# Kernel optimization log

Hardware: AMD Instinct MI355X
Metric: run time of the kernel (lower is better)

Reference implementation:

```python
import jax, jax.numpy as jnp
import numpy as np

TEMP = 1.0  # composition softmax temperature

def _bank_topk(x, U, V, logits, top_k):
    # softmax over primitive logits, select top-k, renormalize, fused low-rank projection
    w = jax.nn.softmax(logits / TEMP)                     # [P]
    tw, ti = jax.lax.top_k(w, top_k)                      # [k], [k]
    tw = tw / tw.sum()
    Us = U[ti]                                            # [k, d_in, r]
    Vs = V[ti]                                            # [k, r, d_out]
    h = jnp.einsum('bsd,kdr->bksr', x, Us)                # low-rank bottleneck
    return jnp.einsum('bksr,kro,k->bso', h, Vs, tw)       # weighted fuse

def reference(x, q_U, q_V, k_U, k_V, v_U, v_V, q_logits, k_logits, v_logits, out_w, top_k):
    B, S, _ = x.shape
    H, D = 16, 64
    q = _bank_topk(x, q_U, q_V, q_logits, top_k)
    k = _bank_topk(x, k_U, k_V, k_logits, top_k)
    v = _bank_topk(x, v_U, v_V, v_logits, top_k)
    q = q.reshape(B, S, H, D).transpose(0, 2, 1, 3)       # [B,H,S,D]
    k = k.reshape(B, S, H, D).transpose(0, 2, 1, 3)
    v = v.reshape(B, S, H, D).transpose(0, 2, 1, 3)
    scale = 1.0 / jnp.sqrt(jnp.asarray(D, dtype=x.dtype))
    scores = jnp.einsum('bhqd,bhkd->bhqk', q, k) * scale  # [B,H,S,S]
    causal = jnp.triu(jnp.ones((S, S), dtype=bool), 1)
    scores = jnp.where(causal[None, None], jnp.finfo(x.dtype).min, scores)
    probs = jax.nn.softmax(scores, axis=-1)
    out = jnp.einsum('bhqk,bhkd->bhqd', probs, v)
    out = out.transpose(0, 2, 1, 3).reshape(B, S, H * D)
    return out @ out_w.T                                   # nn.Linear(H*D, d_model, bias=False)

def setup_inputs() -> dict:
    key = jax.random.key(0)
    ks = jax.random.split(key, 11)
    P, d, r = 16, 1024, 64
    B, S = 4, 1024
    f = jnp.float32
    inp = {
        'x': jax.random.normal(ks[0], (B, S, d), f),
        'q_U': jax.random.normal(ks[1], (P, d, r), f) * (1.0 / np.sqrt(d)),
        'q_V': jax.random.normal(ks[2], (P, r, d), f) * (1.0 / np.sqrt(r)),
        'k_U': jax.random.normal(ks[3], (P, d, r), f) * (1.0 / np.sqrt(d)),
        'k_V': jax.random.normal(ks[4], (P, r, d), f) * (1.0 / np.sqrt(r)),
        'v_U': jax.random.normal(ks[5], (P, d, r), f) * (1.0 / np.sqrt(d)),
        'v_V': jax.random.normal(ks[6], (P, r, d), f) * (1.0 / np.sqrt(r)),
        'q_logits': jax.random.normal(ks[7], (P,), f) * 0.01,
        'k_logits': jax.random.normal(ks[8], (P,), f) * 0.01,
        'v_logits': jax.random.normal(ks[9], (P,), f) * 0.01,
        'out_w': jax.random.normal(ks[10], (d, d), f) * (1.0 / np.sqrt(d)),
        'top_k': 4,
    }
    return inp
```

## Files before the change

### kernel.cpp

```cpp
#include <hip/hip_runtime.h>
#include <math.h>

#define D_MODEL 1024
#define RANK    64
#define PMAX    16
#define S_LEN   1024
#define HD      64
#define MROWS   4096
#define NHEAD   16
#define BATCH   4

typedef short short8v __attribute__((ext_vector_type(8)));
typedef float floatx4 __attribute__((ext_vector_type(4)));

typedef __attribute__((address_space(1))) const unsigned int* gptr_t;
typedef __attribute__((address_space(3))) unsigned int* lptr_t;

static __device__ __forceinline__ void async16(const void* g, void* l) {
    __builtin_amdgcn_global_load_lds((gptr_t)g, (lptr_t)l, 16, 0, 0);
}

static __device__ __forceinline__ short f2bf(float f) {
    unsigned int u = __float_as_uint(f);
    u = (u + 0x7fffu + ((u >> 16) & 1u)) >> 16;
    return (short)u;
}

__global__ void topk_weights_kernel(const float* __restrict__ ql,
                                    const float* __restrict__ kl,
                                    const float* __restrict__ vl,
                                    const int* __restrict__ topk,
                                    int* __restrict__ idx_out,
                                    float* __restrict__ w_out) {
    int bank = threadIdx.x;
    if (bank >= 3) return;
    const float* lg = (bank == 0) ? ql : (bank == 1) ? kl : vl;
    int K = *topk; if (K < 1) K = 1; if (K > PMAX) K = PMAX;
    float l[PMAX];
    for (int i = 0; i < PMAX; ++i) l[i] = lg[i];
    bool used[PMAX];
    for (int i = 0; i < PMAX; ++i) used[i] = false;
    int   sel_i[PMAX];
    float sel_l[PMAX];
    for (int j = 0; j < K; ++j) {
        int best = -1; float bv = -INFINITY;
        for (int i = 0; i < PMAX; ++i)
            if (!used[i] && l[i] > bv) { bv = l[i]; best = i; }
        used[best] = true; sel_i[j] = best; sel_l[j] = bv;
    }
    float mx = sel_l[0];
    float e[PMAX];
    float sum = 0.f;
    for (int j = 0; j < K; ++j) { e[j] = __expf(sel_l[j] - mx); sum += e[j]; }
    float inv = 1.f / sum;
    for (int j = 0; j < PMAX; ++j) {
        idx_out[bank * PMAX + j] = (j < K) ? sel_i[j] : 0;
        w_out[bank * PMAX + j]   = (j < K) ? e[j] * inv : 0.f;
    }
}

__global__ __launch_bounds__(256) void convert_bf16_kernel(
    const float* __restrict__ src, short* __restrict__ dst, int n4) {
    int i = blockIdx.x * 256 + threadIdx.x;
    if (i < n4) {
        float4 f = ((const float4*)src)[i];
        short4 o;
        o.x = f2bf(f.x); o.y = f2bf(f.y); o.z = f2bf(f.z); o.w = f2bf(f.w);
        ((short4*)dst)[i] = o;
    }
}

__global__ __launch_bounds__(256) void prep_uv_kernel(
    const float* __restrict__ qU, const float* __restrict__ kU,
    const float* __restrict__ vU,
    const float* __restrict__ qV, const float* __restrict__ kV,
    const float* __restrict__ vV,
    const int* __restrict__ idx, const float* __restrict__ wsel,
    const int* __restrict__ topk,
    short* __restrict__ Ut, short* __restrict__ Vt) {
    int z    = blockIdx.z;
    int j    = blockIdx.y;
    int tile = blockIdx.x;
    int t    = threadIdx.x;
    int K = *topk; if (K < 1) K = 1; if (K > PMAX) K = PMAX;
    if (j >= K) return;
    __shared__ float T[64][65];
    int bank = (z < 3) ? z : z - 3;
    int p = idx[bank * PMAX + j];

    if (z < 3) {
        const float* U = (bank == 0) ? qU : (bank == 1) ? kU : vU;
        const float* src = U + (size_t)p * D_MODEL * RANK;
        int d0 = tile * 64;
        int rl = t & 63, dq = t >> 6;
#pragma unroll
        for (int i = 0; i < 16; ++i) {
            int dl = i * 4 + dq;
            T[rl][dl] = src[(size_t)(d0 + dl) * RANK + rl];
        }
        __syncthreads();
        short* dst = Ut + (size_t)bank * D_MODEL * D_MODEL;
        int rr = t >> 2;
#pragma unroll
        for (int i = 0; i < 4; ++i) {
            int c = (t & 3) * 16 + i * 4;
            short4 o;
            o.x = f2bf(T[rr][c + 0]); o.y = f2bf(T[rr][c + 1]);
            o.z = f2bf(T[rr][c + 2]); o.w = f2bf(T[rr][c + 3]);
            *(short4*)&dst[(size_t)(j * 64 + rr) * D_MODEL + d0 + c] = o;
        }
    } else {
        const float* V = (bank == 0) ? qV : (bank == 1) ? kV : vV;
        float wj = wsel[bank * PMAX + j];
        const float* src = V + (size_t)p * RANK * D_MODEL;
        int n0 = tile * 64;
        int nl = t & 63, rq = t >> 6;
#pragma unroll
        for (int i = 0; i < 16; ++i) {
            int rl = i * 4 + rq;
            T[nl][rl] = src[(size_t)rl * D_MODEL + n0 + nl] * wj;
        }
        __syncthreads();
        short* dst = Vt + (size_t)bank * D_MODEL * D_MODEL;
        int rr = t >> 2;
#pragma unroll
        for (int i = 0; i < 4; ++i) {
            int c = (t & 3) * 16 + i * 4;
            short4 o;
            o.x = f2bf(T[rr][c + 0]); o.y = f2bf(T[rr][c + 1]);
            o.z = f2bf(T[rr][c + 2]); o.w = f2bf(T[rr][c + 3]);
            *(short4*)&dst[(size_t)(n0 + rr) * D_MODEL + j * 64 + c] = o;
        }
    }
}

static __device__ __forceinline__ void mfma_gemm_tile(
    const short* __restrict__ A, const short* __restrict__ B, int kl,
    int m0, int n0, short* As, short* Bs, floatx4 acc[4][4]) {
    const int t    = threadIdx.x;
    const int w    = t >> 6;
    const int lane = t & 63;
    const int wm   = w & 1, wn = w >> 1;
    const int colL = lane & 15, quad = lane >> 4;
    const int srow  = lane >> 2;
    const int skoff = (lane & 3) * 8;

#pragma unroll
    for (int i = 0; i < 4; ++i)
#pragma unroll
        for (int j = 0; j < 4; ++j) acc[i][j] = (floatx4){0.f, 0.f, 0.f, 0.f};

    for (int k0 = 0; k0 < kl; k0 += 32) {
        async16(A + (size_t)(m0 + w * 16 + srow) * D_MODEL + k0 + skoff,
                As + (w * 16 + srow) * 32 + skoff);
        async16(A + (size_t)(m0 + 64 + w * 16 + srow) * D_MODEL + k0 + skoff,
                As + (64 + w * 16 + srow) * 32 + skoff);
        async16(B + (size_t)(n0 + w * 16 + srow) * D_MODEL + k0 + skoff,
                Bs + (w * 16 + srow) * 32 + skoff);
        async16(B + (size_t)(n0 + 64 + w * 16 + srow) * D_MODEL + k0 + skoff,
                Bs + (64 + w * 16 + srow) * 32 + skoff);
        __syncthreads();
        short8v af[4], bf[4];
#pragma unroll
        for (int i = 0; i < 4; ++i)
            af[i] = *(const short8v*)&As[(wm * 64 + i * 16 + colL) * 32 + quad * 8];
#pragma unroll
        for (int j = 0; j < 4; ++j)
            bf[j] = *(const short8v*)&Bs[(wn * 64 + j * 16 + colL) * 32 + quad * 8];
#pragma unroll
        for (int i = 0; i < 4; ++i)
#pragma unroll
            for (int j = 0; j < 4; ++j)
                acc[i][j] = __builtin_amdgcn_mfma_f32_16x16x32_bf16(af[i], bf[j], acc[i][j], 0, 0, 0);
        __syncthreads();
    }
}

__global__ __launch_bounds__(256) void gemm_h_kernel(
    const short* __restrict__ xb, const short* __restrict__ Ut,
    const int* __restrict__ topk, short* __restrict__ h) {
    int K = *topk; if (K < 1) K = 1; if (K > PMAX) K = PMAX;
    int n0 = blockIdx.y * 128;
    if (n0 >= K * 64) return;
    int m0 = blockIdx.x * 128;
    int bank = blockIdx.z;
    __shared__ short As[128 * 32];
    __shared__ short Bs[128 * 32];
    floatx4 acc[4][4];
    mfma_gemm_tile(xb, Ut + (size_t)bank * D_MODEL * D_MODEL, D_MODEL, m0, n0, As, Bs, acc);

    const int t = threadIdx.x, w = t >> 6, lane = t & 63;
    const int wm = w & 1, wn = w >> 1, colL = lane & 15, quad = lane >> 4;
    short* H = h + (size_t)bank * MROWS * D_MODEL;
#pragma unroll
    for (int i = 0; i < 4; ++i)
#pragma unroll
        for (int j = 0; j < 4; ++j)
#pragma unroll
            for (int r = 0; r < 4; ++r)
                H[(size_t)(m0 + wm * 64 + i * 16 + quad * 4 + r) * D_MODEL +
                  (n0 + wn * 64 + j * 16 + colL)] = f2bf(acc[i][j][r]);
}

__global__ __launch_bounds__(256) void gemm_qkv_kernel(
    const short* __restrict__ h, const short* __restrict__ Vt,
    const int* __restrict__ topk, short* __restrict__ qkv) {
    int K = *topk; if (K < 1) K = 1; if (K > PMAX) K = PMAX;
    int m0 = blockIdx.x * 128;
    int n0 = blockIdx.y * 128;
    int bank = blockIdx.z;
    __shared__ short As[128 * 32];
    __shared__ short Bs[128 * 32];
    floatx4 acc[4][4];
    mfma_gemm_tile(h + (size_t)bank * MROWS * D_MODEL,
                   Vt + (size_t)bank * D_MODEL * D_MODEL, K * 64, m0, n0, As, Bs, acc);

    const int t = threadIdx.x, w = t >> 6, lane = t & 63;
    const int wm = w & 1, wn = w >> 1, colL = lane & 15, quad = lane >> 4;
    short* outp = qkv + (size_t)bank * MROWS * D_MODEL;
#pragma unroll
    for (int i = 0; i < 4; ++i)
#pragma unroll
        for (int j = 0; j < 4; ++j)
#pragma unroll
            for (int r = 0; r < 4; ++r) {
                int m = m0 + wm * 64 + i * 16 + quad * 4 + r;
                int n = n0 + wn * 64 + j * 16 + colL;
                int b = m >> 10, s = m & 1023;
                int head = n >> 6, d = n & 63;
                outp[(((size_t)(b * NHEAD + head) << 10) + s) * HD + d] = f2bf(acc[i][j][r]);
            }
}

__global__ __launch_bounds__(256) void gemm_proj_kernel(
    const short* __restrict__ attnb, const short* __restrict__ wb,
    float* __restrict__ outp) {
    int m0 = blockIdx.x * 128;
    int n0 = blockIdx.y * 128;
    __shared__ short As[128 * 32];
    __shared__ short Bs[128 * 32];
    floatx4 acc[4][4];
    mfma_gemm_tile(attnb, wb, D_MODEL, m0, n0, As, Bs, acc);

    const int t = threadIdx.x, w = t >> 6, lane = t & 63;
    const int wm = w & 1, wn = w >> 1, colL = lane & 15, quad = lane >> 4;
#pragma unroll
    for (int i = 0; i < 4; ++i)
#pragma unroll
        for (int j = 0; j < 4; ++j)
#pragma unroll
            for (int r = 0; r < 4; ++r)
                outp[(size_t)(m0 + wm * 64 + i * 16 + quad * 4 + r) * D_MODEL +
                     (n0 + wn * 64 + j * 16 + colL)] = acc[i][j][r];
}

__global__ __launch_bounds__(256) void attn_mfma_kernel(
    const short* __restrict__ qkv,
    short* __restrict__ attn_out) {
    const int t    = threadIdx.x;
    const int w    = t >> 6;
    const int lane = t & 63;
    const int col  = lane & 15;
    const int quad = lane >> 4;
    const int pr   = blockIdx.x;
    const int bh   = blockIdx.y;
    const size_t HS   = (size_t)S_LEN * HD;
    const size_t BSTR = (size_t)MROWS * D_MODEL;
    const short* Qg = qkv + (size_t)bh * HS;
    const short* Kg = qkv + BSTR + (size_t)bh * HS;
    const short* Vg = qkv + 2 * BSTR + (size_t)bh * HS;

    __shared__ short Ks[64][72];
    __shared__ short Vt[64][72];
    __shared__ short Ps[4][16][72];

    const float SC = 0.125f * 1.44269504f;

    for (int ph = 0; ph < 2; ++ph) {
        const int qt = ph ? (15 - pr) : pr;
        const int qrow = qt * 64 + w * 16 + col;
        short8v aq0 = *(const short8v*)(Qg + (size_t)qrow * HD + quad * 8);
        short8v aq1 = *(const short8v*)(Qg + (size_t)qrow * HD + 32 + quad * 8);
        floatx4 O0 = {0.f, 0.f, 0.f, 0.f}, O1 = O0, O2 = O0, O3 = O0;
        float mrow[4] = {-INFINITY, -INFINITY, -INFINITY, -INFINITY};
        float lrow[4] = {0.f, 0.f, 0.f, 0.f};

        for (int jt = 0; jt <= qt; ++jt) {
            __syncthreads();
            {
                int c = t;
                int key = c >> 3, db = (c & 7) * 8;
                *(short8v*)&Ks[key][db] =
                    *(const short8v*)(Kg + (size_t)(jt * 64 + key) * HD + db);
                c = t + 256;
                key = c >> 3; db = (c & 7) * 8;
                *(short8v*)&Ks[key][db] =
                    *(const short8v*)(Kg + (size_t)(jt * 64 + key) * HD + db);
            }
            {
                int k0 = (t & 31) * 2;
                int db = (t >> 5) * 8;
                short8v v0 = *(const short8v*)(Vg + (size_t)(jt * 64 + k0) * HD + db);
                short8v v1 = *(const short8v*)(Vg + (size_t)(jt * 64 + k0 + 1) * HD + db);
#pragma unroll
                for (int i = 0; i < 8; ++i) {
                    unsigned int pk = (unsigned int)(unsigned short)v0[i] |
                                      ((unsigned int)(unsigned short)v1[i] << 16);
                    *(unsigned int*)&Vt[db + i][k0] = pk;
                }
            }
            __syncthreads();

            const bool diag = (jt == qt);
            const int  nmax = diag ? w : 3;
            float sc[4][4];
#pragma unroll
            for (int n = 0; n < 4; ++n) {
                if (n <= nmax) {
                    floatx4 c4 = {0.f, 0.f, 0.f, 0.f};
                    short8v b0 = *(const short8v*)&Ks[n * 16 + col][quad * 8];
                    short8v b1 = *(const short8v*)&Ks[n * 16 + col][32 + quad * 8];
                    c4 = __builtin_amdgcn_mfma_f32_16x16x32_bf16(aq0, b0, c4, 0, 0, 0);
                    c4 = __builtin_amdgcn_mfma_f32_16x16x32_bf16(aq1, b1, c4, 0, 0, 0);
#pragma unroll
                    for (int r = 0; r < 4; ++r) {
                        float v = c4[r] * SC;
                        if (diag && n == w && col > quad * 4 + r) v = -INFINITY;
                        sc[n][r] = v;
                    }
                } else {
#pragma unroll
                    for (int r = 0; r < 4; ++r) sc[n][r] = -INFINITY;
                }
            }
            float pv[4][4];
#pragma unroll
            for (int r = 0; r < 4; ++r) {
                float tm = fmaxf(fmaxf(sc[0][r], sc[1][r]), fmaxf(sc[2][r], sc[3][r]));
                tm = fmaxf(tm, __shfl_xor(tm, 1));
                tm = fmaxf(tm, __shfl_xor(tm, 2));
                tm = fmaxf(tm, __shfl_xor(tm, 4));
                tm = fmaxf(tm, __shfl_xor(tm, 8));
                float mnew  = fmaxf(mrow[r], tm);
                float alpha = exp2f(mrow[r] - mnew);
                float ps = 0.f;
#pragma unroll
                for (int n = 0; n < 4; ++n) {
                    float p = exp2f(sc[n][r] - mnew);
                    pv[n][r] = p;
                    ps += p;
                }
                ps += __shfl_xor(ps, 1);
                ps += __shfl_xor(ps, 2);
                ps += __shfl_xor(ps, 4);
                ps += __shfl_xor(ps, 8);
                lrow[r] = lrow[r] * alpha + ps;
                mrow[r] = mnew;
                O0[r] *= alpha; O1[r] *= alpha; O2[r] *= alpha; O3[r] *= alpha;
            }
#pragma unroll
            for (int n = 0; n < 4; ++n)
#pragma unroll
                for (int r = 0; r < 4; ++r)
                    Ps[w][quad * 4 + r][n * 16 + col] = f2bf(pv[n][r]);
            const int ksmax = diag ? (w >> 1) : 1;
#pragma unroll
            for (int ks = 0; ks < 2; ++ks) {
                if (ks > ksmax) break;
                short8v ap  = *(const short8v*)&Ps[w][col][ks * 32 + quad * 8];
                short8v bv0 = *(const short8v*)&Vt[0  + col][ks * 32 + quad * 8];
                short8v bv1 = *(const short8v*)&Vt[16 + col][ks * 32 + quad * 8];
                short8v bv2 = *(const short8v*)&Vt[32 + col][ks * 32 + quad * 8];
                short8v bv3 = *(const short8v*)&Vt[48 + col][ks * 32 + quad * 8];
                O0 = __builtin_amdgcn_mfma_f32_16x16x32_bf16(ap, bv0, O0, 0, 0, 0);
                O1 = __builtin_amdgcn_mfma_f32_16x16x32_bf16(ap, bv1, O1, 0, 0, 0);
                O2 = __builtin_amdgcn_mfma_f32_16x16x32_bf16(ap, bv2, O2, 0, 0, 0);
                O3 = __builtin_amdgcn_mfma_f32_16x16x32_bf16(ap, bv3, O3, 0, 0, 0);
            }
        }
        const int b  = bh >> 4;
        const int hh = bh & 15;
        short* orow = attn_out +
            ((size_t)(b * S_LEN) + qt * 64 + w * 16) * D_MODEL + hh * 64;
#pragma unroll
        for (int r = 0; r < 4; ++r) {
            float inv = 1.f / lrow[r];
            short* prw = orow + (size_t)(quad * 4 + r) * D_MODEL;
            prw[0  + col] = f2bf(O0[r] * inv);
            prw[16 + col] = f2bf(O1[r] * inv);
            prw[32 + col] = f2bf(O2[r] * inv);
            prw[48 + col] = f2bf(O3[r] * inv);
        }
    }
}

extern "C" void kernel_launch(void* const* d_in, const int* in_sizes, int n_in,
                              void* d_out, int out_size, void* d_ws, size_t ws_size,
                              hipStream_t stream) {
    const float* x    = (const float*)d_in[0];
    const float* qU   = (const float*)d_in[1];
    const float* qV   = (const float*)d_in[2];
    const float* kU   = (const float*)d_in[3];
    const float* kV   = (const float*)d_in[4];
    const float* vU   = (const float*)d_in[5];
    const float* vV   = (const float*)d_in[6];
    const float* qlg  = (const float*)d_in[7];
    const float* klg  = (const float*)d_in[8];
    const float* vlg  = (const float*)d_in[9];
    const float* outw = (const float*)d_in[10];
    const int*   topk = (const int*)d_in[11];
    float* outp = (float*)d_out;

    char* ws = (char*)d_ws;
    int*   idxp = (int*)ws;
    float* wp   = (float*)(ws + 256);
    short* xb   = (short*)(ws + 512);
    short* Ut   = xb + (size_t)MROWS * D_MODEL;
    short* Vt   = Ut + (size_t)3 * D_MODEL * D_MODEL;
    short* wb   = Vt + (size_t)3 * D_MODEL * D_MODEL;
    short* hbuf = wb + (size_t)D_MODEL * D_MODEL;
    short* qkvb = hbuf + (size_t)3 * MROWS * D_MODEL;
    short* attnb = qkvb + (size_t)3 * MROWS * D_MODEL;

    topk_weights_kernel<<<1, 64, 0, stream>>>(qlg, klg, vlg, topk, idxp, wp);
    convert_bf16_kernel<<<(MROWS * D_MODEL / 4 + 255) / 256, 256, 0, stream>>>(
        x, xb, MROWS * D_MODEL / 4);
    convert_bf16_kernel<<<(D_MODEL * D_MODEL / 4 + 255) / 256, 256, 0, stream>>>(
        outw, wb, D_MODEL * D_MODEL / 4);
    prep_uv_kernel<<<dim3(16, 16, 6), 256, 0, stream>>>(
        qU, kU, vU, qV, kV, vV, idxp, wp, topk, Ut, Vt);
    gemm_h_kernel<<<dim3(32, 8, 3), 256, 0, stream>>>(xb, Ut, topk, hbuf);
    gemm_qkv_kernel<<<dim3(32, 8, 3), 256, 0, stream>>>(hbuf, Vt, topk, qkvb);
    attn_mfma_kernel<<<dim3(8, 64), 256, 0, stream>>>(qkvb, attnb);
    gemm_proj_kernel<<<dim3(32, 8), 256, 0, stream>>>(attnb, wb, outp);
}
```

Baseline: 227.2 us.

## Precompute effective weights V^T·U^T per bank and schedule attention one tile per block

Instead of computing h = x·U and then h·V over 4096 rows, the code first forms an effective d×d weight matrix W = V^T U^T per bank (a small 1024×1024×256 GEMM) and then runs a single x·W GEMM to get q/k/v. This removes the intermediate h buffer and its write/read traffic, but the qkv GEMM now always runs the full K=1024 instead of K=256, which adds FLOPs. The attention kernel also drops the paired-query-tile loop and launches one block per query tile (16×64 grid), processing heaviest tiles first. That doubles the block count and should help load balancing.

```diff
diff --git a/kernel.cpp b/kernel.cpp
--- a/kernel.cpp
+++ b/kernel.cpp
@@ -9,6 +9,7 @@
 #define MROWS   4096
 #define NHEAD   16
 #define BATCH   4
+#define KCMAX   (PMAX * RANK)
 
 typedef short short8v __attribute__((ext_vector_type(8)));
 typedef float floatx4 __attribute__((ext_vector_type(4)));
@@ -77,7 +78,7 @@
     const float* __restrict__ vV,
     const int* __restrict__ idx, const float* __restrict__ wsel,
     const int* __restrict__ topk,
-    short* __restrict__ Ut, short* __restrict__ Vt) {
+    short* __restrict__ Uc, short* __restrict__ Vt) {
     int z    = blockIdx.z;
     int j    = blockIdx.y;
     int tile = blockIdx.x;
@@ -91,23 +92,16 @@
     if (z < 3) {
         const float* U = (bank == 0) ? qU : (bank == 1) ? kU : vU;
         const float* src = U + (size_t)p * D_MODEL * RANK;
-        int d0 = tile * 64;
-        int rl = t & 63, dq = t >> 6;
-#pragma unroll
-        for (int i = 0; i < 16; ++i) {
-            int dl = i * 4 + dq;
-            T[rl][dl] = src[(size_t)(d0 + dl) * RANK + rl];
-        }
-        __syncthreads();
-        short* dst = Ut + (size_t)bank * D_MODEL * D_MODEL;
-        int rr = t >> 2;
+        short* dst = Uc + (size_t)bank * D_MODEL * KCMAX;
+        int r4 = (t & 15) * 4;
+        int dl = t >> 4;
 #pragma unroll
         for (int i = 0; i < 4; ++i) {
-            int c = (t & 3) * 16 + i * 4;
+            int d = tile * 64 + i * 16 + dl;
+            float4 f = *(const float4*)&src[(size_t)d * RANK + r4];
             short4 o;
-            o.x = f2bf(T[rr][c + 0]); o.y = f2bf(T[rr][c + 1]);
-            o.z = f2bf(T[rr][c + 2]); o.w = f2bf(T[rr][c + 3]);
-            *(short4*)&dst[(size_t)(j * 64 + rr) * D_MODEL + d0 + c] = o;
+            o.x = f2bf(f.x); o.y = f2bf(f.y); o.z = f2bf(f.z); o.w = f2bf(f.w);
+            *(short4*)&dst[(size_t)d * KCMAX + j * 64 + r4] = o;
         }
     } else {
         const float* V = (bank == 0) ? qV : (bank == 1) ? kV : vV;
@@ -121,7 +115,7 @@
             T[nl][rl] = src[(size_t)rl * D_MODEL + n0 + nl] * wj;
         }
         __syncthreads();
-        short* dst = Vt + (size_t)bank * D_MODEL * D_MODEL;
+        short* dst = Vt + (size_t)bank * D_MODEL * KCMAX;
         int rr = t >> 2;
 #pragma unroll
         for (int i = 0; i < 4; ++i) {
@@ -129,14 +123,14 @@
             short4 o;
             o.x = f2bf(T[rr][c + 0]); o.y = f2bf(T[rr][c + 1]);
             o.z = f2bf(T[rr][c + 2]); o.w = f2bf(T[rr][c + 3]);
-            *(short4*)&dst[(size_t)(n0 + rr) * D_MODEL + j * 64 + c] = o;
+            *(short4*)&dst[(size_t)(n0 + rr) * KCMAX + j * 64 + c] = o;
         }
     }
 }
 
 static __device__ __forceinline__ void mfma_gemm_tile(
     const short* __restrict__ A, const short* __restrict__ B, int kl,
-    int m0, int n0, short* As, short* Bs, floatx4 acc[4][4]) {
+    int lda, int ldb, int m0, int n0, short* As, short* Bs, floatx4 acc[4][4]) {
     const int t    = threadIdx.x;
     const int w    = t >> 6;
     const int lane = t & 63;
@@ -151,13 +145,13 @@
         for (int j = 0; j < 4; ++j) acc[i][j] = (floatx4){0.f, 0.f, 0.f, 0.f};
 
     for (int k0 = 0; k0 < kl; k0 += 32) {
-        async16(A + (size_t)(m0 + w * 16 + srow) * D_MODEL + k0 + skoff,
+        async16(A + (size_t)(m0 + w * 16 + srow) * lda + k0 + skoff,
                 As + (w * 16 + srow) * 32 + skoff);
-        async16(A + (size_t)(m0 + 64 + w * 16 + srow) * D_MODEL + k0 + skoff,
+        async16(A + (size_t)(m0 + 64 + w * 16 + srow) * lda + k0 + skoff,
                 As + (64 + w * 16 + srow) * 32 + skoff);
-        async16(B + (size_t)(n0 + w * 16 + srow) * D_MODEL + k0 + skoff,
+        async16(B + (size_t)(n0 + w * 16 + srow) * ldb + k0 + skoff,
                 Bs + (w * 16 + srow) * 32 + skoff);
-        async16(B + (size_t)(n0 + 64 + w * 16 + srow) * D_MODEL + k0 + skoff,
+        async16(B + (size_t)(n0 + 64 + w * 16 + srow) * ldb + k0 + skoff,
                 Bs + (64 + w * 16 + srow) * 32 + skoff);
         __syncthreads();
         short8v af[4], bf[4];
@@ -176,35 +170,9 @@
     }
 }
 
-__global__ __launch_bounds__(256) void gemm_h_kernel(
-    const short* __restrict__ xb, const short* __restrict__ Ut,
-    const int* __restrict__ topk, short* __restrict__ h) {
-    int K = *topk; if (K < 1) K = 1; if (K > PMAX) K = PMAX;
-    int n0 = blockIdx.y * 128;
-    if (n0 >= K * 64) return;
-    int m0 = blockIdx.x * 128;
-    int bank = blockIdx.z;
-    __shared__ short As[128 * 32];
-    __shared__ short Bs[128 * 32];
-    floatx4 acc[4][4];
-    mfma_gemm_tile(xb, Ut + (size_t)bank * D_MODEL * D_MODEL, D_MODEL, m0, n0, As, Bs, acc);
-
-    const int t = threadIdx.x, w = t >> 6, lane = t & 63;
-    const int wm = w & 1, wn = w >> 1, colL = lane & 15, quad = lane >> 4;
-    short* H = h + (size_t)bank * MROWS * D_MODEL;
-#pragma unroll
-    for (int i = 0; i < 4; ++i)
-#pragma unroll
-        for (int j = 0; j < 4; ++j)
-#pragma unroll
-            for (int r = 0; r < 4; ++r)
-                H[(size_t)(m0 + wm * 64 + i * 16 + quad * 4 + r) * D_MODEL +
-                  (n0 + wn * 64 + j * 16 + colL)] = f2bf(acc[i][j][r]);
-}
-
-__global__ __launch_bounds__(256) void gemm_qkv_kernel(
-    const short* __restrict__ h, const short* __restrict__ Vt,
-    const int* __restrict__ topk, short* __restrict__ qkv) {
+__global__ __launch_bounds__(256) void gemm_weff_kernel(
+    const short* __restrict__ Vt, const short* __restrict__ Uc,
+    const int* __restrict__ topk, short* __restrict__ Wt) {
     int K = *topk; if (K < 1) K = 1; if (K > PMAX) K = PMAX;
     int m0 = blockIdx.x * 128;
     int n0 = blockIdx.y * 128;
@@ -212,8 +180,34 @@
     __shared__ short As[128 * 32];
     __shared__ short Bs[128 * 32];
     floatx4 acc[4][4];
-    mfma_gemm_tile(h + (size_t)bank * MROWS * D_MODEL,
-                   Vt + (size_t)bank * D_MODEL * D_MODEL, K * 64, m0, n0, As, Bs, acc);
+    mfma_gemm_tile(Vt + (size_t)bank * D_MODEL * KCMAX,
+                   Uc + (size_t)bank * D_MODEL * KCMAX,
+                   K * 64, KCMAX, KCMAX, m0, n0, As, Bs, acc);
+
+    const int t = threadIdx.x, w = t >> 6, lane = t & 63;
+    const int wm = w & 1, wn = w >> 1, colL = lane & 15, quad = lane >> 4;
+    short* Wb = Wt + (size_t)bank * D_MODEL * D_MODEL;
+#pragma unroll
+    for (int i = 0; i < 4; ++i)
+#pragma unroll
+        for (int j = 0; j < 4; ++j)
+#pragma unroll
+            for (int r = 0; r < 4; ++r)
+                Wb[(size_t)(m0 + wm * 64 + i * 16 + quad * 4 + r) * D_MODEL +
+                   (n0 + wn * 64 + j * 16 + colL)] = f2bf(acc[i][j][r]);
+}
+
+__global__ __launch_bounds__(256) void gemm_qkv_kernel(
+    const short* __restrict__ xb, const short* __restrict__ Wt,
+    short* __restrict__ qkv) {
+    int m0 = blockIdx.x * 128;
+    int n0 = blockIdx.y * 128;
+    int bank = blockIdx.z;
+    __shared__ short As[128 * 32];
+    __shared__ short Bs[128 * 32];
+    floatx4 acc[4][4];
+    mfma_gemm_tile(xb, Wt + (size_t)bank * D_MODEL * D_MODEL,
+                   D_MODEL, D_MODEL, D_MODEL, m0, n0, As, Bs, acc);
 
     const int t = threadIdx.x, w = t >> 6, lane = t & 63;
     const int wm = w & 1, wn = w >> 1, colL = lane & 15, quad = lane >> 4;
@@ -240,7 +234,7 @@
     __shared__ short As[128 * 32];
     __shared__ short Bs[128 * 32];
     floatx4 acc[4][4];
-    mfma_gemm_tile(attnb, wb, D_MODEL, m0, n0, As, Bs, acc);
+    mfma_gemm_tile(attnb, wb, D_MODEL, D_MODEL, D_MODEL, m0, n0, As, Bs, acc);
 
     const int t = threadIdx.x, w = t >> 6, lane = t & 63;
     const int wm = w & 1, wn = w >> 1, colL = lane & 15, quad = lane >> 4;
@@ -262,7 +256,7 @@
     const int lane = t & 63;
     const int col  = lane & 15;
     const int quad = lane >> 4;
-    const int pr   = blockIdx.x;
+    const int qt   = 15 - (int)blockIdx.x;
     const int bh   = blockIdx.y;
     const size_t HS   = (size_t)S_LEN * HD;
     const size_t BSTR = (size_t)MROWS * D_MODEL;
@@ -276,121 +270,118 @@
 
     const float SC = 0.125f * 1.44269504f;
 
-    for (int ph = 0; ph < 2; ++ph) {
-        const int qt = ph ? (15 - pr) : pr;
-        const int qrow = qt * 64 + w * 16 + col;
-        short8v aq0 = *(const short8v*)(Qg + (size_t)qrow * HD + quad * 8);
-        short8v aq1 = *(const short8v*)(Qg + (size_t)qrow * HD + 32 + quad * 8);
-        floatx4 O0 = {0.f, 0.f, 0.f, 0.f}, O1 = O0, O2 = O0, O3 = O0;
-        float mrow[4] = {-INFINITY, -INFINITY, -INFINITY, -INFINITY};
-        float lrow[4] = {0.f, 0.f, 0.f, 0.f};
-
-        for (int jt = 0; jt <= qt; ++jt) {
-            __syncthreads();
-            {
-                int c = t;
-                int key = c >> 3, db = (c & 7) * 8;
-                *(short8v*)&Ks[key][db] =
-                    *(const short8v*)(Kg + (size_t)(jt * 64 + key) * HD + db);
-                c = t + 256;
-                key = c >> 3; db = (c & 7) * 8;
-                *(short8v*)&Ks[key][db] =
-                    *(const short8v*)(Kg + (size_t)(jt * 64 + key) * HD + db);
+    const int qrow = qt * 64 + w * 16 + col;
+    short8v aq0 = *(const short8v*)(Qg + (size_t)qrow * HD + quad * 8);
+    short8v aq1 = *(const short8v*)(Qg + (size_t)qrow * HD + 32 + quad * 8);
+    floatx4 O0 = {0.f, 0.f, 0.f, 0.f}, O1 = O0, O2 = O0, O3 = O0;
+    float mrow[4] = {-INFINITY, -INFINITY, -INFINITY, -INFINITY};
+    float lrow[4] = {0.f, 0.f, 0.f, 0.f};
+
+    for (int jt = 0; jt <= qt; ++jt) {
+        __syncthreads();
+        {
+            int c = t;
+            int key = c >> 3, db = (c & 7) * 8;
+            *(short8v*)&Ks[key][db] =
+                *(const short8v*)(Kg + (size_t)(jt * 64 + key) * HD + db);
+            c = t + 256;
+            key = c >> 3; db = (c & 7) * 8;
+            *(short8v*)&Ks[key][db] =
+                *(const short8v*)(Kg + (size_t)(jt * 64 + key) * HD + db);
+        }
+        {
+            int k0 = (t & 31) * 2;
+            int db = (t >> 5) * 8;
+            short8v v0 = *(const short8v*)(Vg + (size_t)(jt * 64 + k0) * HD + db);
+            short8v v1 = *(const short8v*)(Vg + (size_t)(jt * 64 + k0 + 1) * HD + db);
+#pragma unroll
+            for (int i = 0; i < 8; ++i) {
+                unsigned int pk = (unsigned int)(unsigned short)v0[i] |
+                                  ((unsigned int)(unsigned short)v1[i] << 16);
+                *(unsigned int*)&Vt[db + i][k0] = pk;
             }
-            {
-                int k0 = (t & 31) * 2;
-                int db = (t >> 5) * 8;
-                short8v v0 = *(const short8v*)(Vg + (size_t)(jt * 64 + k0) * HD + db);
-                short8v v1 = *(const short8v*)(Vg + (size_t)(jt * 64 + k0 + 1) * HD + db);
-#pragma unroll
-                for (int i = 0; i < 8; ++i) {
-                    unsigned int pk = (unsigned int)(unsigned short)v0[i] |
-                                      ((unsigned int)(unsigned short)v1[i] << 16);
-                    *(unsigned int*)&Vt[db + i][k0] = pk;
+        }
+        __syncthreads();
+
+        const bool diag = (jt == qt);
+        const int  nmax = diag ? w : 3;
+        float sc[4][4];
+#pragma unroll
+        for (int n = 0; n < 4; ++n) {
+            if (n <= nmax) {
+                floatx4 c4 = {0.f, 0.f, 0.f, 0.f};
+                short8v b0 = *(const short8v*)&Ks[n * 16 + col][quad * 8];
+                short8v b1 = *(const short8v*)&Ks[n * 16 + col][32 + quad * 8];
+                c4 = __builtin_amdgcn_mfma_f32_16x16x32_bf16(aq0, b0, c4, 0, 0, 0);
+                c4 = __builtin_amdgcn_mfma_f32_16x16x32_bf16(aq1, b1, c4, 0, 0, 0);
+#pragma unroll
+                for (int r = 0; r < 4; ++r) {
+                    float v = c4[r] * SC;
+                    if (diag && n == w && col > quad * 4 + r) v = -INFINITY;
+                    sc[n][r] = v;
                 }
+            } else {
+#pragma unroll
+                for (int r = 0; r < 4; ++r) sc[n][r] = -INFINITY;
             }
-            __syncthreads();
-
-            const bool diag = (jt == qt);
-            const int  nmax = diag ? w : 3;
-            float sc[4][4];
+        }
+        float pv[4][4];
+#pragma unroll
+        for (int r = 0; r < 4; ++r) {
+            float tm = fmaxf(fmaxf(sc[0][r], sc[1][r]), fmaxf(sc[2][r], sc[3][r]));
+            tm = fmaxf(tm, __shfl_xor(tm, 1));
+            tm = fmaxf(tm, __shfl_xor(tm, 2));
+            tm = fmaxf(tm, __shfl_xor(tm, 4));
+            tm = fmaxf(tm, __shfl_xor(tm, 8));
+            float mnew  = fmaxf(mrow[r], tm);
+            float alpha = exp2f(mrow[r] - mnew);
+            float ps = 0.f;
 #pragma unroll
             for (int n = 0; n < 4; ++n) {
-                if (n <= nmax) {
-                    floatx4 c4 = {0.f, 0.f, 0.f, 0.f};
-                    short8v b0 = *(const short8v*)&Ks[n * 16 + col][quad * 8];
-                    short8v b1 = *(const short8v*)&Ks[n * 16 + col][32 + quad * 8];
-                    c4 = __builtin_amdgcn_mfma_f32_16x16x32_bf16(aq0, b0, c4, 0, 0, 0);
-                    c4 = __builtin_amdgcn_mfma_f32_16x16x32_bf16(aq1, b1, c4, 0, 0, 0);
-#pragma unroll
-                    for (int r = 0; r < 4; ++r) {
-                        float v = c4[r] * SC;
-                        if (diag && n == w && col > quad * 4 + r) v = -INFINITY;
-                        sc[n][r] = v;
-                    }
-                } else {
-#pragma unroll
-                    for (int r = 0; r < 4; ++r) sc[n][r] = -INFINITY;
-                }
+                float p = exp2f(sc[n][r] - mnew);
+                pv[n][r] = p;
+                ps += p;
             }
-            float pv[4][4];
-#pragma unroll
-            for (int r = 0; r < 4; ++r) {
-                float tm = fmaxf(fmaxf(sc[0][r], sc[1][r]), fmaxf(sc[2][r], sc[3][r]));
-                tm = fmaxf(tm, __shfl_xor(tm, 1));
-                tm = fmaxf(tm, __shfl_xor(tm, 2));
-                tm = fmaxf(tm, __shfl_xor(tm, 4));
-                tm = fmaxf(tm, __shfl_xor(tm, 8));
-                float mnew  = fmaxf(mrow[r], tm);
-                float alpha = exp2f(mrow[r] - mnew);
-                float ps = 0.f;
-#pragma unroll
-                for (int n = 0; n < 4; ++n) {
-                    float p = exp2f(sc[n][r] - mnew);
-                    pv[n][r] = p;
-                    ps += p;
-                }
-                ps += __shfl_xor(ps, 1);
-                ps += __shfl_xor(ps, 2);
-                ps += __shfl_xor(ps, 4);
-                ps += __shfl_xor(ps, 8);
-                lrow[r] = lrow[r] * alpha + ps;
-                mrow[r] = mnew;
-                O0[r] *= alpha; O1[r] *= alpha; O2[r] *= alpha; O3[r] *= alpha;
-            }
-#pragma unroll
-            for (int n = 0; n < 4; ++n)
-#pragma unroll
-                for (int r = 0; r < 4; ++r)
-                    Ps[w][quad * 4 + r][n * 16 + col] = f2bf(pv[n][r]);
-            const int ksmax = diag ? (w >> 1) : 1;
-#pragma unroll
-            for (int ks = 0; ks < 2; ++ks) {
-                if (ks > ksmax) break;
-                short8v ap  = *(const short8v*)&Ps[w][col][ks * 32 + quad * 8];
-                short8v bv0 = *(const short8v*)&Vt[0  + col][ks * 32 + quad * 8];
-                short8v bv1 = *(const short8v*)&Vt[16 + col][ks * 32 + quad * 8];
-                short8v bv2 = *(const short8v*)&Vt[32 + col][ks * 32 + quad * 8];
-                short8v bv3 = *(const short8v*)&Vt[48 + col][ks * 32 + quad * 8];
-                O0 = __builtin_amdgcn_mfma_f32_16x16x32_bf16(ap, bv0, O0, 0, 0, 0);
-                O1 = __builtin_amdgcn_mfma_f32_16x16x32_bf16(ap, bv1, O1, 0, 0, 0);
-                O2 = __builtin_amdgcn_mfma_f32_16x16x32_bf16(ap, bv2, O2, 0, 0, 0);
-                O3 = __builtin_amdgcn_mfma_f32_16x16x32_bf16(ap, bv3, O3, 0, 0, 0);
-            }
-        }
-        const int b  = bh >> 4;
-        const int hh = bh & 15;
-        short* orow = attn_out +
-            ((size_t)(b * S_LEN) + qt * 64 + w * 16) * D_MODEL + hh * 64;
-#pragma unroll
-        for (int r = 0; r < 4; ++r) {
-            float inv = 1.f / lrow[r];
-            short* prw = orow + (size_t)(quad * 4 + r) * D_MODEL;
-            prw[0  + col] = f2bf(O0[r] * inv);
-            prw[16 + col] = f2bf(O1[r] * inv);
-            prw[32 + col] = f2bf(O2[r] * inv);
-            prw[48 + col] = f2bf(O3[r] * inv);
-        }
+            ps += __shfl_xor(ps, 1);
+            ps += __shfl_xor(ps, 2);
+            ps += __shfl_xor(ps, 4);
+            ps += __shfl_xor(ps, 8);
+            lrow[r] = lrow[r] * alpha + ps;
+            mrow[r] = mnew;
+            O0[r] *= alpha; O1[r] *= alpha; O2[r] *= alpha; O3[r] *= alpha;
+        }
+#pragma unroll
+        for (int n = 0; n < 4; ++n)
+#pragma unroll
+            for (int r = 0; r < 4; ++r)
+                Ps[w][quad * 4 + r][n * 16 + col] = f2bf(pv[n][r]);
+        const int ksmax = diag ? (w >> 1) : 1;
+#pragma unroll
+        for (int ks = 0; ks < 2; ++ks) {
+            if (ks > ksmax) break;
+            short8v ap  = *(const short8v*)&Ps[w][col][ks * 32 + quad * 8];
+            short8v bv0 = *(const short8v*)&Vt[0  + col][ks * 32 + quad * 8];
+            short8v bv1 = *(const short8v*)&Vt[16 + col][ks * 32 + quad * 8];
+            short8v bv2 = *(const short8v*)&Vt[32 + col][ks * 32 + quad * 8];
+            short8v bv3 = *(const short8v*)&Vt[48 + col][ks * 32 + quad * 8];
+            O0 = __builtin_amdgcn_mfma_f32_16x16x32_bf16(ap, bv0, O0, 0, 0, 0);
+            O1 = __builtin_amdgcn_mfma_f32_16x16x32_bf16(ap, bv1, O1, 0, 0, 0);
+            O2 = __builtin_amdgcn_mfma_f32_16x16x32_bf16(ap, bv2, O2, 0, 0, 0);
+            O3 = __builtin_amdgcn_mfma_f32_16x16x32_bf16(ap, bv3, O3, 0, 0, 0);
+        }
+    }
+    const int b  = bh >> 4;
+    const int hh = bh & 15;
+    short* orow = attn_out +
+        ((size_t)(b * S_LEN) + qt * 64 + w * 16) * D_MODEL + hh * 64;
+#pragma unroll
+    for (int r = 0; r < 4; ++r) {
+        float inv = 1.f / lrow[r];
+        short* prw = orow + (size_t)(quad * 4 + r) * D_MODEL;
+        prw[0  + col] = f2bf(O0[r] * inv);
+        prw[16 + col] = f2bf(O1[r] * inv);
+        prw[32 + col] = f2bf(O2[r] * inv);
+        prw[48 + col] = f2bf(O3[r] * inv);
     }
 }
 
@@ -415,11 +406,11 @@
     int*   idxp = (int*)ws;
     float* wp   = (float*)(ws + 256);
     short* xb   = (short*)(ws + 512);
-    short* Ut   = xb + (size_t)MROWS * D_MODEL;
-    short* Vt   = Ut + (size_t)3 * D_MODEL * D_MODEL;
-    short* wb   = Vt + (size_t)3 * D_MODEL * D_MODEL;
-    short* hbuf = wb + (size_t)D_MODEL * D_MODEL;
-    short* qkvb = hbuf + (size_t)3 * MROWS * D_MODEL;
+    short* Uc   = xb + (size_t)MROWS * D_MODEL;
+    short* Vt   = Uc + (size_t)3 * D_MODEL * KCMAX;
+    short* wb   = Vt + (size_t)3 * D_MODEL * KCMAX;
+    short* Wt   = wb + (size_t)D_MODEL * D_MODEL;
+    short* qkvb = Wt + (size_t)3 * D_MODEL * D_MODEL;
     short* attnb = qkvb + (size_t)3 * MROWS * D_MODEL;
 
     topk_weights_kernel<<<1, 64, 0, stream>>>(qlg, klg, vlg, topk, idxp, wp);
@@ -428,9 +419,9 @@
     convert_bf16_kernel<<<(D_MODEL * D_MODEL / 4 + 255) / 256, 256, 0, stream>>>(
         outw, wb, D_MODEL * D_MODEL / 4);
     prep_uv_kernel<<<dim3(16, 16, 6), 256, 0, stream>>>(
-        qU, kU, vU, qV, kV, vV, idxp, wp, topk, Ut, Vt);
-    gemm_h_kernel<<<dim3(32, 8, 3), 256, 0, stream>>>(xb, Ut, topk, hbuf);
-    gemm_qkv_kernel<<<dim3(32, 8, 3), 256, 0, stream>>>(hbuf, Vt, topk, qkvb);
-    attn_mfma_kernel<<<dim3(8, 64), 256, 0, stream>>>(qkvb, attnb);
+        qU, kU, vU, qV, kV, vV, idxp, wp, topk, Uc, Vt);
+    gemm_weff_kernel<<<dim3(8, 8, 3), 256, 0, stream>>>(Vt, Uc, topk, Wt);
+    gemm_qkv_kernel<<<dim3(32, 8, 3), 256, 0, stream>>>(xb, Wt, qkvb);
+    attn_mfma_kernel<<<dim3(16, 64), 256, 0, stream>>>(qkvb, attnb);
     gemm_proj_kernel<<<dim3(32, 8), 256, 0, stream>>>(attnb, wb, outp);
 }
```

New measurement: 243.3 us. 1.07x slower.
